# Performance work log

Hardware: AMD Instinct MI355X
Metric: run time of the kernel (lower is better)

Reference implementation:

```python
import jax, jax.numpy as jnp
import numpy as np

N_NODES = 100000
N_EDGES = 1600000
DIM = 128          # feat_dim == hidden_dim
N_LAYERS = 3
N_GRAPHS = 128
BN_EPS = 1e-5


def setup_inputs() -> dict:
    key = jax.random.key(0)
    ks = jax.random.split(key, 10)
    x = jax.random.normal(ks[0], (N_NODES, DIM), dtype=jnp.float32)
    edge_index = jax.random.randint(ks[1], (2, N_EDGES), 0, N_NODES, dtype=jnp.int32)
    batch = jnp.sort(jax.random.randint(ks[2], (N_NODES,), 0, N_GRAPHS, dtype=jnp.int32))
    # Xavier-uniform MLP weights (Linear stored as [in, out]); biases zero-init per module.
    a = float(np.sqrt(6.0 / (DIM + DIM)))
    W1 = jax.random.uniform(ks[3], (N_LAYERS, DIM, DIM), jnp.float32, -a, a)
    b1 = jnp.zeros((N_LAYERS, DIM), jnp.float32)
    W2 = jax.random.uniform(ks[4], (N_LAYERS, DIM, DIM), jnp.float32, -a, a)
    b2 = jnp.zeros((N_LAYERS, DIM), jnp.float32)
    gamma = jnp.ones((N_LAYERS, DIM), jnp.float32)   # BatchNorm weight
    beta = jnp.zeros((N_LAYERS, DIM), jnp.float32)   # BatchNorm bias
    return {"x": x, "edge_index": edge_index, "batch": batch,
            "W1": W1, "b1": b1, "W2": W2, "b2": b2, "gamma": gamma, "beta": beta}


def reference(x, edge_index, batch, W1, b1, W2, b2, gamma, beta):
    n_nodes = x.shape[0]
    src, dst = edge_index[0], edge_index[1]
    h = x
    xs = []
    for i in range(N_LAYERS):
        # GINConv (eps=0): h_i <- MLP((1+eps)*h_i + sum_{j->i} h_j)
        agg = jax.ops.segment_sum(h[src], dst, num_segments=n_nodes)
        z = h + agg
        z = jax.nn.relu(z @ W1[i] + b1[i]) @ W2[i] + b2[i]
        z = jax.nn.relu(z)
        # BatchNorm1d, training mode: biased batch stats over node dim
        mu = jnp.mean(z, axis=0)
        var = jnp.var(z, axis=0)
        h = gamma[i] * (z - mu) * jax.lax.rsqrt(var + BN_EPS) + beta[i]
        xs.append(h)
    # global_add_pool per layer output, concatenated over feature dim
    xpool = [jax.ops.segment_sum(xi, batch, num_segments=N_GRAPHS) for xi in xs]
    global_rep = jnp.concatenate(xpool, axis=1)  # [N_GRAPHS, N_LAYERS*DIM]
    return (global_rep, h)
```

## Files before the change

### kernel.cpp

```cpp
#include <hip/hip_runtime.h>

#define DIM 128
#define NLAYERS 3
#define NGRAPHS 128
#define BN_EPS 1e-5f
#define NSTAT 32

typedef __attribute__((ext_vector_type(8))) short short8v;
typedef __attribute__((ext_vector_type(8))) unsigned short ushort8v;
typedef __attribute__((ext_vector_type(4))) float f32x4;

__device__ __forceinline__ unsigned short f2bf(float f) {
  unsigned int x = __float_as_uint(f);
  unsigned int r = (x + 0x7fffu + ((x >> 16) & 1u)) >> 16;
  return (unsigned short)r;
}
__device__ __forceinline__ float bflo(unsigned int u) { return __uint_as_float(u << 16); }
__device__ __forceinline__ float bfhi(unsigned int u) { return __uint_as_float(u & 0xffff0000u); }
__device__ __forceinline__ float bf2f(unsigned short u) {
  return __uint_as_float(((unsigned int)u) << 16);
}


#define P1CH 4096

__global__ __launch_bounds__(256) void p1_kernel(const int* __restrict__ src,
                                                 const int* __restrict__ dst,
                                                 int* __restrict__ bucketCursor,
                                                 unsigned int* __restrict__ pairs,
                                                 int stride, int E, int NB) {
  __shared__ int cnt[128];
  __shared__ int base[128];
  int t = threadIdx.x;
  int e0 = blockIdx.x * P1CH;
  int e1 = min(e0 + P1CH, E);
  if (t < NB) cnt[t] = 0;
  __syncthreads();
  for (int e = e0 + t; e < e1; e += 256) atomicAdd(&cnt[dst[e] >> 10], 1);
  __syncthreads();
  if (t < NB) {
    base[t] = atomicAdd(&bucketCursor[t], cnt[t]);
    cnt[t] = 0;
  }
  __syncthreads();
  for (int e = e0 + t; e < e1; e += 256) {
    int d = dst[e];
    int b = d >> 10;
    int p = atomicAdd(&cnt[b], 1) + base[b];
    pairs[(size_t)b * stride + p] = ((unsigned int)(d & 1023) << 20) | (unsigned int)src[e];
  }
}

__global__ __launch_bounds__(128) void bscan2_kernel(const int* __restrict__ bucketCursor,
                                                     int* __restrict__ bucketBase,
                                                     int* __restrict__ offsets, int NB, int N) {
  __shared__ int p[128];
  int t = threadIdx.x;
  p[t] = (t < NB) ? bucketCursor[t] : 0;
  __syncthreads();
  for (int off = 1; off < 128; off <<= 1) {
    int v = (t >= off) ? p[t - off] : 0;
    __syncthreads();
    p[t] += v;
    __syncthreads();
  }
  if (t < NB) bucketBase[t] = (t == 0) ? 0 : p[t - 1];
  if (t == 0) offsets[N] = p[127];
}

__global__ __launch_bounds__(1024) void p2_kernel(const unsigned int* __restrict__ pairs,
                                                  const int* __restrict__ bucketCursor,
                                                  const int* __restrict__ bucketBase,
                                                  int stride, int* __restrict__ offsets,
                                                  int* __restrict__ eidx, int N) {
  __shared__ int cur[1024];
  int b = blockIdx.x;
  int t = threadIdx.x;
  int sz = bucketCursor[b];
  int ebase = bucketBase[b];
  const unsigned int* pp = pairs + (size_t)b * stride;
  cur[t] = 0;
  __syncthreads();
  for (int i = t; i < sz; i += 1024) atomicAdd(&cur[pp[i] >> 20], 1);
  __syncthreads();
  int v = cur[t];
  __syncthreads();
  cur[t] = v;
  __syncthreads();
  for (int off = 1; off < 1024; off <<= 1) {
    int u = (t >= off) ? cur[t - off] : 0;
    __syncthreads();
    cur[t] += u;
    __syncthreads();
  }
  int excl = cur[t] - v;
  int node = b * 1024 + t;
  if (node < N) offsets[node] = ebase + excl;
  cur[t] = excl;
  __syncthreads();
  for (int i = t; i < sz; i += 1024) {
    unsigned int pv = pp[i];
    int p = atomicAdd(&cur[pv >> 20], 1);
    eidx[ebase + p] = (int)(pv & 0xFFFFFu);
  }
}


__global__ __launch_bounds__(256) void convx_kernel(const float* __restrict__ x,
                                                    unsigned short* __restrict__ out,
                                                    int nquads) {
  int i = blockIdx.x * 256 + threadIdx.x;
  if (i < nquads) {
    float4 v = ((const float4*)x)[i];
    ushort4 o;
    o.x = f2bf(v.x); o.y = f2bf(v.y); o.z = f2bf(v.z); o.w = f2bf(v.w);
    ((ushort4*)out)[i] = o;
  }
}

__global__ __launch_bounds__(256) void convw_kernel(const float* __restrict__ W1,
                                                    const float* __restrict__ W2,
                                                    unsigned short* __restrict__ Wt) {
  int m = blockIdx.x;
  const float* W = (m < 3) ? (W1 + (size_t)m * 16384) : (W2 + (size_t)(m - 3) * 16384);
  unsigned short* out = Wt + (size_t)m * 16384;
  __shared__ unsigned short t[128 * 130];
  for (int i = threadIdx.x; i < 16384; i += 256) {
    int k = i >> 7, n = i & 127;
    t[n * 130 + k] = f2bf(W[i]);
  }
  __syncthreads();
  for (int i = threadIdx.x; i < 16384; i += 256) {
    int n = i >> 7, k = i & 127;
    out[i] = t[n * 130 + k];
  }
}

__global__ __launch_bounds__(128) void cnt_kernel(const int* __restrict__ batch,
                                                  int* __restrict__ cntG, int N) {
  int g = threadIdx.x;
  int lo = 0, hi = N;
  while (lo < hi) { int mid = (lo + hi) >> 1; if (batch[mid] < g) lo = mid + 1; else hi = mid; }
  int a = lo;
  lo = 0; hi = N;
  while (lo < hi) { int mid = (lo + hi) >> 1; if (batch[mid] < g + 1) lo = mid + 1; else hi = mid; }
  cntG[g] = lo - a;
}


__global__ __launch_bounds__(128) void bnfold_kernel(const float* __restrict__ statsRaw,
                                                     const float* __restrict__ gammaL,
                                                     const float* __restrict__ betaL,
                                                     float invN, float* __restrict__ folded) {
  int d = threadIdx.x;
  float s = 0.f, q = 0.f;
#pragma unroll
  for (int k = 0; k < NSTAT; ++k) {
    s += statsRaw[k * 256 + d];
    q += statsRaw[k * 256 + 128 + d];
  }
  float mu = s * invN;
  float var = q * invN - mu * mu;
  float sc = gammaL[d] * rsqrtf(var + BN_EPS);
  folded[d] = sc;
  folded[128 + d] = betaL[d] - mu * sc;
}


__global__ __launch_bounds__(256) void agg_kernel(const unsigned short* __restrict__ uin,
                                                  const int* __restrict__ offsets,
                                                  const int* __restrict__ eidx,
                                                  unsigned short* __restrict__ zout,
                                                  const float* __restrict__ foldedPrev,
                                                  int isFirst, int N) {
  int wid = (blockIdx.x * 256 + threadIdx.x) >> 6;
  int lane = threadIdx.x & 63;
  if (wid >= N) return;
  float scx = 1.f, scy = 1.f, shx = 0.f, shy = 0.f;
  if (!isFirst) {
    int d0 = lane * 2;
    float2 scv = *(const float2*)&foldedPrev[d0];
    float2 shv = *(const float2*)&foldedPrev[128 + d0];
    scx = scv.x; scy = scv.y; shx = shv.x; shy = shv.y;
  }
  const unsigned int* h32 = (const unsigned int*)uin;
  unsigned int own = h32[(size_t)wid * 64 + lane];
  float ax = bflo(own), ay = bfhi(own);
  int beg = offsets[wid], end = offsets[wid + 1];
  int e = beg;
  for (; e + 7 < end; e += 8) {
    int s0 = eidx[e], s1 = eidx[e + 1], s2 = eidx[e + 2], s3 = eidx[e + 3];
    int s4 = eidx[e + 4], s5 = eidx[e + 5], s6 = eidx[e + 6], s7 = eidx[e + 7];
    unsigned int u0 = h32[(size_t)s0 * 64 + lane];
    unsigned int u1 = h32[(size_t)s1 * 64 + lane];
    unsigned int u2 = h32[(size_t)s2 * 64 + lane];
    unsigned int u3 = h32[(size_t)s3 * 64 + lane];
    unsigned int u4 = h32[(size_t)s4 * 64 + lane];
    unsigned int u5 = h32[(size_t)s5 * 64 + lane];
    unsigned int u6 = h32[(size_t)s6 * 64 + lane];
    unsigned int u7 = h32[(size_t)s7 * 64 + lane];
    ax += bflo(u0) + bflo(u1) + bflo(u2) + bflo(u3);
    ay += bfhi(u0) + bfhi(u1) + bfhi(u2) + bfhi(u3);
    ax += bflo(u4) + bflo(u5) + bflo(u6) + bflo(u7);
    ay += bfhi(u4) + bfhi(u5) + bfhi(u6) + bfhi(u7);
  }
  for (; e + 1 < end; e += 2) {
    int s0 = eidx[e], s1 = eidx[e + 1];
    unsigned int u0 = h32[(size_t)s0 * 64 + lane];
    unsigned int u1 = h32[(size_t)s1 * 64 + lane];
    ax += bflo(u0) + bflo(u1);
    ay += bfhi(u0) + bfhi(u1);
  }
  if (e < end) {
    unsigned int u0 = h32[(size_t)eidx[e] * 64 + lane];
    ax += bflo(u0);
    ay += bfhi(u0);
  }
  float degp1 = (float)(end - beg + 1);
  float zx = scx * ax + degp1 * shx;
  float zy = scy * ay + degp1 * shy;
  unsigned int packed = (unsigned int)f2bf(zx) | ((unsigned int)f2bf(zy) << 16);
  ((unsigned int*)zout)[(size_t)wid * 64 + lane] = packed;
}


__global__ __launch_bounds__(256) void mlp_pool_kernel(unsigned short* __restrict__ zio,
                                                       const int* __restrict__ batch,
                                                       const unsigned short* __restrict__ WtA,
                                                       const float* __restrict__ b1,
                                                       const unsigned short* __restrict__ WtB,
                                                       const float* __restrict__ b2,
                                                       float* __restrict__ statsCur,
                                                       float* __restrict__ poolU,
                                                       int poolcol, int N) {
  __shared__ unsigned short tt[64 * 136];
  __shared__ float sstat[256];
  __shared__ int batchLDS[64];
  const int tid = threadIdx.x;
  const int n0 = blockIdx.x * 64;
  const int w = tid >> 6;
  const int lane = tid & 63;
  const int l15 = lane & 15;
  const int eslot = lane >> 4;
  const int hi8 = eslot << 3;
  sstat[tid] = 0.f;
  if (tid < 64) batchLDS[tid] = (n0 + tid < N) ? batch[n0 + tid] : 0;
  __syncthreads();

  const int arow = n0 + w * 16 + l15;
  const bool avalid = arow < N;

  f32x4 acc[8];
#pragma unroll
  for (int nf = 0; nf < 8; ++nf) acc[nf] = (f32x4){0.f, 0.f, 0.f, 0.f};
#pragma unroll
  for (int kt = 0; kt < 4; ++kt) {
    int kk = kt * 32 + hi8;
    short8v a0 = {0, 0, 0, 0, 0, 0, 0, 0};
    if (avalid) a0 = *(const short8v*)&zio[(size_t)arow * 128 + kk];
#pragma unroll
    for (int nf = 0; nf < 8; ++nf) {
      short8v b = *(const short8v*)&WtA[(size_t)(nf * 16 + l15) * 128 + kk];
      acc[nf] = __builtin_amdgcn_mfma_f32_16x16x32_bf16(a0, b, acc[nf], 0, 0, 0);
    }
  }
#pragma unroll
  for (int nf = 0; nf < 8; ++nf) {
    float bv = b1[nf * 16 + l15];
    int col = nf * 16 + l15;
#pragma unroll
    for (int q = 0; q < 4; ++q) {
      int row = w * 16 + eslot * 4 + q;
      tt[row * 136 + col] = f2bf(fmaxf(acc[nf][q] + bv, 0.f));
    }
  }

#pragma unroll
  for (int nf = 0; nf < 8; ++nf) acc[nf] = (f32x4){0.f, 0.f, 0.f, 0.f};
#pragma unroll
  for (int kt = 0; kt < 4; ++kt) {
    int kk = kt * 32 + hi8;
    short8v a0 = *(const short8v*)&tt[(w * 16 + l15) * 136 + kk];
#pragma unroll
    for (int nf = 0; nf < 8; ++nf) {
      short8v b = *(const short8v*)&WtB[(size_t)(nf * 16 + l15) * 128 + kk];
      acc[nf] = __builtin_amdgcn_mfma_f32_16x16x32_bf16(a0, b, acc[nf], 0, 0, 0);
    }
  }

#pragma unroll
  for (int nf = 0; nf < 8; ++nf) {
    float bv = b2[nf * 16 + l15];
    int col = nf * 16 + l15;
    float sv = 0.f, sq = 0.f;
#pragma unroll
    for (int q = 0; q < 4; ++q) {
      int row = w * 16 + eslot * 4 + q;
      float u = fmaxf(acc[nf][q] + bv, 0.f);
      tt[row * 136 + col] = f2bf(u);
      float um = ((n0 + row) < N) ? u : 0.f;
      sv += um;
      sq += um * um;
    }
    sv += __shfl_xor(sv, 16); sv += __shfl_xor(sv, 32);
    sq += __shfl_xor(sq, 16); sq += __shfl_xor(sq, 32);
    if (lane < 16) {
      atomicAdd(&sstat[col], sv);
      atomicAdd(&sstat[128 + col], sq);
    }
  }

  for (int i = lane; i < 256; i += 64) {
    int r = w * 16 + (i >> 4), c8 = (i & 15) << 3;
    int node = n0 + r;
    if (node < N)
      *(ushort8v*)&zio[(size_t)node * 128 + c8] = *(const ushort8v*)&tt[r * 136 + c8];
  }
  __syncthreads();

  float* myStat = statsCur + ((blockIdx.x & (NSTAT - 1)) << 8);
  atomicAdd(&myStat[tid], sstat[tid]);
  int d = tid & 127, half = tid >> 7;
  int curg = -1;
  float accp = 0.f;
  for (int r = half; r < 64; r += 2) {
    if (n0 + r >= N) break;
    float uv = bf2f(tt[r * 136 + d]);
    int g = batchLDS[r];
    if (g != curg) {
      if (curg >= 0) atomicAdd(&poolU[(size_t)curg * (NLAYERS * DIM) + poolcol + d], accp);
      curg = g;
      accp = 0.f;
    }
    accp += uv;
  }
  if (curg >= 0) atomicAdd(&poolU[(size_t)curg * (NLAYERS * DIM) + poolcol + d], accp);
}


__global__ __launch_bounds__(256) void hwrite_kernel(const unsigned short* __restrict__ u,
                                                     const float* __restrict__ folded,
                                                     float* __restrict__ hout, int N) {
  __shared__ float scs[128], shs[128];
  if (threadIdx.x < 128) {
    scs[threadIdx.x] = folded[threadIdx.x];
    shs[threadIdx.x] = folded[128 + threadIdx.x];
  }
  __syncthreads();
  int i = blockIdx.x * 256 + threadIdx.x;
  if (i >= N * 16) return;
  int row = i >> 4, c8 = (i & 15) << 3;
  ushort8v v = *(const ushort8v*)&u[(size_t)row * 128 + c8];
  float4 o0, o1;
  o0.x = scs[c8 + 0] * bf2f((unsigned short)v[0]) + shs[c8 + 0];
  o0.y = scs[c8 + 1] * bf2f((unsigned short)v[1]) + shs[c8 + 1];
  o0.z = scs[c8 + 2] * bf2f((unsigned short)v[2]) + shs[c8 + 2];
  o0.w = scs[c8 + 3] * bf2f((unsigned short)v[3]) + shs[c8 + 3];
  o1.x = scs[c8 + 4] * bf2f((unsigned short)v[4]) + shs[c8 + 4];
  o1.y = scs[c8 + 5] * bf2f((unsigned short)v[5]) + shs[c8 + 5];
  o1.z = scs[c8 + 6] * bf2f((unsigned short)v[6]) + shs[c8 + 6];
  o1.w = scs[c8 + 7] * bf2f((unsigned short)v[7]) + shs[c8 + 7];
  *(float4*)&hout[(size_t)row * 128 + c8] = o0;
  *(float4*)&hout[(size_t)row * 128 + c8 + 4] = o1;
}


__global__ __launch_bounds__(384) void pfin_kernel(const float* __restrict__ poolU,
                                                   const float* __restrict__ folded,
                                                   const int* __restrict__ cntG,
                                                   float* __restrict__ pool) {
  int g = blockIdx.x;
  int c = threadIdx.x;
  int L = c >> 7, d = c & 127;
  float sc = folded[L * 256 + d];
  float sh = folded[L * 256 + 128 + d];
  pool[(size_t)g * 384 + c] = sc * poolU[(size_t)g * 384 + c] + (float)cntG[g] * sh;
}


extern "C" void kernel_launch(void* const* d_in, const int* in_sizes, int n_in,
                              void* d_out, int out_size, void* d_ws, size_t ws_size,
                              hipStream_t stream) {
  const float* x = (const float*)d_in[0];
  const int* edge = (const int*)d_in[1];
  const int* batch = (const int*)d_in[2];
  const float* W1 = (const float*)d_in[3];
  const float* b1 = (const float*)d_in[4];
  const float* W2 = (const float*)d_in[5];
  const float* b2 = (const float*)d_in[6];
  const float* gamma = (const float*)d_in[7];
  const float* beta = (const float*)d_in[8];

  int N = in_sizes[0] / DIM;
  int E = in_sizes[1] / 2;
  const int* src = edge;
  const int* dst = edge + E;
  int NB = (N + 1023) >> 10;
  int stride = E / NB + E / (NB * 4) + 2048;

  const int statsSz = NLAYERS * NSTAT * 256;
  char* w = (char*)d_ws;
  int* eidx = (int*)w;                w += sizeof(int) * (size_t)E;
  int* offsets = (int*)w;             w += sizeof(int) * (size_t)(N + 8);
  int* bucketCursor = (int*)w;        w += sizeof(int) * 128;
  int* bucketBase = (int*)w;          w += sizeof(int) * 128;
  float* gstats = (float*)w;          w += sizeof(float) * statsSz;
  float* folded = (float*)w;          w += sizeof(float) * NLAYERS * 256;
  float* poolU = (float*)w;           w += sizeof(float) * (size_t)NGRAPHS * NLAYERS * DIM;
  int* cntG = (int*)w;                w += sizeof(int) * 128;
  unsigned short* Wt = (unsigned short*)w;  w += sizeof(short) * 6 * 16384;
  uintptr_t a = ((uintptr_t)w + 255) & ~(uintptr_t)255;
  unsigned short* bufA = (unsigned short*)a;
  unsigned short* bufB = bufA + (size_t)N * 128;
  unsigned int* pairs = (unsigned int*)bufA;

  float* pool = (float*)d_out;
  float* hout = (float*)d_out + (size_t)NGRAPHS * NLAYERS * DIM;

  hipMemsetAsync(bucketCursor, 0, 128 * sizeof(int), stream);
  hipMemsetAsync(gstats, 0,
                 (statsSz + NLAYERS * 256 + (size_t)NGRAPHS * NLAYERS * DIM) * sizeof(float),
                 stream);

  convw_kernel<<<6, 256, 0, stream>>>(W1, W2, Wt);
  convx_kernel<<<(N * DIM / 4 + 255) / 256, 256, 0, stream>>>(x, bufB, N * DIM / 4);

  p1_kernel<<<(E + P1CH - 1) / P1CH, 256, 0, stream>>>(src, dst, bucketCursor, pairs,
                                                       stride, E, NB);
  bscan2_kernel<<<1, 128, 0, stream>>>(bucketCursor, bucketBase, offsets, NB, N);
  p2_kernel<<<NB, 1024, 0, stream>>>(pairs, bucketCursor, bucketBase, stride, offsets,
                                     eidx, N);
  cnt_kernel<<<1, 128, 0, stream>>>(batch, cntG, N);

  float invN = 1.0f / (float)N;
  int ablk = (N + 3) / 4;
  int mblk = (N + 63) / 64;
  float* st0 = gstats;
  float* st1 = gstats + NSTAT * 256;
  float* st2 = gstats + 2 * NSTAT * 256;

  agg_kernel<<<ablk, 256, 0, stream>>>(bufB, offsets, eidx, bufA, folded, 1, N);
  mlp_pool_kernel<<<mblk, 256, 0, stream>>>(bufA, batch, Wt + 0 * 16384, b1 + 0,
                                            Wt + 3 * 16384, b2 + 0, st0, poolU, 0, N);
  bnfold_kernel<<<1, 128, 0, stream>>>(st0, gamma + 0, beta + 0, invN, folded + 0);
  agg_kernel<<<ablk, 256, 0, stream>>>(bufA, offsets, eidx, bufB, folded + 0, 0, N);
  mlp_pool_kernel<<<mblk, 256, 0, stream>>>(bufB, batch, Wt + 1 * 16384, b1 + 128,
                                            Wt + 4 * 16384, b2 + 128, st1, poolU, 128, N);
  bnfold_kernel<<<1, 128, 0, stream>>>(st1, gamma + 128, beta + 128, invN, folded + 256);
  agg_kernel<<<ablk, 256, 0, stream>>>(bufB, offsets, eidx, bufA, folded + 256, 0, N);
  mlp_pool_kernel<<<mblk, 256, 0, stream>>>(bufA, batch, Wt + 2 * 16384, b1 + 256,
                                            Wt + 5 * 16384, b2 + 256, st2, poolU, 256, N);
  bnfold_kernel<<<1, 128, 0, stream>>>(st2, gamma + 256, beta + 256, invN, folded + 512);

  hwrite_kernel<<<(N * 16 + 255) / 256, 256, 0, stream>>>(bufA, folded + 512, hout, N);
  pfin_kernel<<<NGRAPHS, 384, 0, stream>>>(poolU, folded, cntG, pool);
}
```

Baseline: 519.0 us.

## Split MLP into per-wave 64-row GEMM kernel and separate pool/stats kernel

The fused MLP+pool kernel is split in two. The GEMM kernel gives each wave 64 rows and holds the weight fragments in registers across four row tiles, so weight loads are reused instead of reloaded per 16 rows. A separate kernel then reads the bf16 output back to compute the BatchNorm statistics and the graph pooling, and the stats slot count is doubled to reduce atomic contention. This costs one extra launch and an extra full read of the activations per layer, and the larger accumulator array raises register pressure.

```diff
diff --git a/kernel.cpp b/kernel.cpp
--- a/kernel.cpp
+++ b/kernel.cpp
@@ -4,7 +4,7 @@
 #define NLAYERS 3
 #define NGRAPHS 128
 #define BN_EPS 1e-5f
-#define NSTAT 32
+#define NSTAT 64
 
 typedef __attribute__((ext_vector_type(8))) short short8v;
 typedef __attribute__((ext_vector_type(8))) unsigned short ushort8v;
@@ -224,117 +224,149 @@
 }
 
 
-__global__ __launch_bounds__(256) void mlp_pool_kernel(unsigned short* __restrict__ zio,
-                                                       const int* __restrict__ batch,
+__global__ __launch_bounds__(128) void mlp_gemm_kernel(unsigned short* __restrict__ zio,
                                                        const unsigned short* __restrict__ WtA,
                                                        const float* __restrict__ b1,
                                                        const unsigned short* __restrict__ WtB,
-                                                       const float* __restrict__ b2,
-                                                       float* __restrict__ statsCur,
-                                                       float* __restrict__ poolU,
-                                                       int poolcol, int N) {
-  __shared__ unsigned short tt[64 * 136];
-  __shared__ float sstat[256];
-  __shared__ int batchLDS[64];
+                                                       const float* __restrict__ b2, int N) {
+  __shared__ unsigned short tt[2][64 * 136];
   const int tid = threadIdx.x;
-  const int n0 = blockIdx.x * 64;
-  const int w = tid >> 6;
+  const int wv = tid >> 6;
   const int lane = tid & 63;
   const int l15 = lane & 15;
   const int eslot = lane >> 4;
-  const int hi8 = eslot << 3;
-  sstat[tid] = 0.f;
-  if (tid < 64) batchLDS[tid] = (n0 + tid < N) ? batch[n0 + tid] : 0;
-  __syncthreads();
-
-  const int arow = n0 + w * 16 + l15;
-  const bool avalid = arow < N;
-
-  f32x4 acc[8];
-#pragma unroll
-  for (int nf = 0; nf < 8; ++nf) acc[nf] = (f32x4){0.f, 0.f, 0.f, 0.f};
-#pragma unroll
+  const int wid = blockIdx.x * 2 + wv;
+  const int n0 = wid * 64;
+  if (n0 >= N) return;
+  unsigned short* t = tt[wv];
+
+  f32x4 acc[4][8];
+#pragma unroll
+  for (int rt = 0; rt < 4; ++rt)
+#pragma unroll
+    for (int nf = 0; nf < 8; ++nf) acc[rt][nf] = (f32x4){0.f, 0.f, 0.f, 0.f};
   for (int kt = 0; kt < 4; ++kt) {
-    int kk = kt * 32 + hi8;
-    short8v a0 = {0, 0, 0, 0, 0, 0, 0, 0};
-    if (avalid) a0 = *(const short8v*)&zio[(size_t)arow * 128 + kk];
+    int kk = kt * 32 + eslot * 8;
+    short8v b[8];
+#pragma unroll
+    for (int nf = 0; nf < 8; ++nf)
+      b[nf] = *(const short8v*)&WtA[(size_t)(nf * 16 + l15) * 128 + kk];
+#pragma unroll
+    for (int rt = 0; rt < 4; ++rt) {
+      int arow = n0 + rt * 16 + l15;
+      short8v a = {0, 0, 0, 0, 0, 0, 0, 0};
+      if (arow < N) a = *(const short8v*)&zio[(size_t)arow * 128 + kk];
+#pragma unroll
+      for (int nf = 0; nf < 8; ++nf)
+        acc[rt][nf] = __builtin_amdgcn_mfma_f32_16x16x32_bf16(a, b[nf], acc[rt][nf], 0, 0, 0);
+    }
+  }
+#pragma unroll
+  for (int rt = 0; rt < 4; ++rt)
 #pragma unroll
     for (int nf = 0; nf < 8; ++nf) {
-      short8v b = *(const short8v*)&WtA[(size_t)(nf * 16 + l15) * 128 + kk];
-      acc[nf] = __builtin_amdgcn_mfma_f32_16x16x32_bf16(a0, b, acc[nf], 0, 0, 0);
+      float bv = b1[nf * 16 + l15];
+      int col = nf * 16 + l15;
+#pragma unroll
+      for (int q = 0; q < 4; ++q) {
+        int row = rt * 16 + eslot * 4 + q;
+        t[row * 136 + col] = f2bf(fmaxf(acc[rt][nf][q] + bv, 0.f));
+      }
     }
-  }
-#pragma unroll
-  for (int nf = 0; nf < 8; ++nf) {
-    float bv = b1[nf * 16 + l15];
-    int col = nf * 16 + l15;
-#pragma unroll
-    for (int q = 0; q < 4; ++q) {
-      int row = w * 16 + eslot * 4 + q;
-      tt[row * 136 + col] = f2bf(fmaxf(acc[nf][q] + bv, 0.f));
+
+#pragma unroll
+  for (int rt = 0; rt < 4; ++rt)
+#pragma unroll
+    for (int nf = 0; nf < 8; ++nf) acc[rt][nf] = (f32x4){0.f, 0.f, 0.f, 0.f};
+  for (int kt = 0; kt < 4; ++kt) {
+    int kk = kt * 32 + eslot * 8;
+    short8v b[8];
+#pragma unroll
+    for (int nf = 0; nf < 8; ++nf)
+      b[nf] = *(const short8v*)&WtB[(size_t)(nf * 16 + l15) * 128 + kk];
+#pragma unroll
+    for (int rt = 0; rt < 4; ++rt) {
+      short8v a = *(const short8v*)&t[(rt * 16 + l15) * 136 + kk];
+#pragma unroll
+      for (int nf = 0; nf < 8; ++nf)
+        acc[rt][nf] = __builtin_amdgcn_mfma_f32_16x16x32_bf16(a, b[nf], acc[rt][nf], 0, 0, 0);
     }
   }
-
-#pragma unroll
-  for (int nf = 0; nf < 8; ++nf) acc[nf] = (f32x4){0.f, 0.f, 0.f, 0.f};
-#pragma unroll
-  for (int kt = 0; kt < 4; ++kt) {
-    int kk = kt * 32 + hi8;
-    short8v a0 = *(const short8v*)&tt[(w * 16 + l15) * 136 + kk];
+#pragma unroll
+  for (int rt = 0; rt < 4; ++rt)
 #pragma unroll
     for (int nf = 0; nf < 8; ++nf) {
-      short8v b = *(const short8v*)&WtB[(size_t)(nf * 16 + l15) * 128 + kk];
-      acc[nf] = __builtin_amdgcn_mfma_f32_16x16x32_bf16(a0, b, acc[nf], 0, 0, 0);
+      float bv = b2[nf * 16 + l15];
+      int col = nf * 16 + l15;
+#pragma unroll
+      for (int q = 0; q < 4; ++q) {
+        int row = rt * 16 + eslot * 4 + q;
+        t[row * 136 + col] = f2bf(fmaxf(acc[rt][nf][q] + bv, 0.f));
+      }
     }
-  }
-
-#pragma unroll
-  for (int nf = 0; nf < 8; ++nf) {
-    float bv = b2[nf * 16 + l15];
-    int col = nf * 16 + l15;
-    float sv = 0.f, sq = 0.f;
-#pragma unroll
-    for (int q = 0; q < 4; ++q) {
-      int row = w * 16 + eslot * 4 + q;
-      float u = fmaxf(acc[nf][q] + bv, 0.f);
-      tt[row * 136 + col] = f2bf(u);
-      float um = ((n0 + row) < N) ? u : 0.f;
-      sv += um;
-      sq += um * um;
-    }
-    sv += __shfl_xor(sv, 16); sv += __shfl_xor(sv, 32);
-    sq += __shfl_xor(sq, 16); sq += __shfl_xor(sq, 32);
-    if (lane < 16) {
-      atomicAdd(&sstat[col], sv);
-      atomicAdd(&sstat[128 + col], sq);
-    }
-  }
-
-  for (int i = lane; i < 256; i += 64) {
-    int r = w * 16 + (i >> 4), c8 = (i & 15) << 3;
+
+  for (int i = lane; i < 1024; i += 64) {
+    int r = i >> 4, c8 = (i & 15) << 3;
     int node = n0 + r;
     if (node < N)
-      *(ushort8v*)&zio[(size_t)node * 128 + c8] = *(const ushort8v*)&tt[r * 136 + c8];
-  }
-  __syncthreads();
-
-  float* myStat = statsCur + ((blockIdx.x & (NSTAT - 1)) << 8);
-  atomicAdd(&myStat[tid], sstat[tid]);
-  int d = tid & 127, half = tid >> 7;
+      *(ushort8v*)&zio[(size_t)node * 128 + c8] = *(const ushort8v*)&t[r * 136 + c8];
+  }
+}
+
+
+__global__ __launch_bounds__(256) void pool_stats_kernel(const unsigned short* __restrict__ u,
+                                                         const int* __restrict__ batch,
+                                                         float* __restrict__ statsCur,
+                                                         float* __restrict__ poolU,
+                                                         int poolcol, int N) {
+  __shared__ float sstat[512];
+  __shared__ int batchLDS[128];
+  const int tid = threadIdx.x;
+  const int n0 = blockIdx.x * 128;
+  sstat[tid] = 0.f;
+  sstat[tid + 256] = 0.f;
+  if (tid < 128) batchLDS[tid] = (n0 + tid < N) ? batch[n0 + tid] : 0;
+  __syncthreads();
+
+  const int dh = tid & 63;
+  const int rg = tid >> 6;
+  const int dp = dh * 2;
+  const unsigned int* u32p = (const unsigned int*)u;
+  float s0 = 0.f, s1 = 0.f, q0 = 0.f, q1 = 0.f;
   int curg = -1;
-  float accp = 0.f;
-  for (int r = half; r < 64; r += 2) {
-    if (n0 + r >= N) break;
-    float uv = bf2f(tt[r * 136 + d]);
+  float a0 = 0.f, a1 = 0.f;
+  for (int r = rg; r < 128; r += 4) {
+    int node = n0 + r;
+    if (node >= N) break;
+    unsigned int v = u32p[(size_t)node * 64 + dh];
+    float x0 = bflo(v), x1 = bfhi(v);
+    s0 += x0; s1 += x1;
+    q0 += x0 * x0; q1 += x1 * x1;
     int g = batchLDS[r];
     if (g != curg) {
-      if (curg >= 0) atomicAdd(&poolU[(size_t)curg * (NLAYERS * DIM) + poolcol + d], accp);
+      if (curg >= 0) {
+        atomicAdd(&poolU[(size_t)curg * (NLAYERS * DIM) + poolcol + dp], a0);
+        atomicAdd(&poolU[(size_t)curg * (NLAYERS * DIM) + poolcol + dp + 1], a1);
+      }
       curg = g;
-      accp = 0.f;
+      a0 = 0.f; a1 = 0.f;
     }
-    accp += uv;
-  }
-  if (curg >= 0) atomicAdd(&poolU[(size_t)curg * (NLAYERS * DIM) + poolcol + d], accp);
+    a0 += x0; a1 += x1;
+  }
+  if (curg >= 0) {
+    atomicAdd(&poolU[(size_t)curg * (NLAYERS * DIM) + poolcol + dp], a0);
+    atomicAdd(&poolU[(size_t)curg * (NLAYERS * DIM) + poolcol + dp + 1], a1);
+  }
+  atomicAdd(&sstat[dp], s0);
+  atomicAdd(&sstat[dp + 1], s1);
+  atomicAdd(&sstat[256 + dp], q0);
+  atomicAdd(&sstat[256 + dp + 1], q1);
+  __syncthreads();
+  float* myStat = statsCur + ((blockIdx.x & (NSTAT - 1)) << 8);
+  if (tid < 128) {
+    atomicAdd(&myStat[tid], sstat[tid]);
+    atomicAdd(&myStat[128 + tid], sstat[256 + tid]);
+  }
 }
 
 
@@ -434,22 +466,26 @@
 
   float invN = 1.0f / (float)N;
   int ablk = (N + 3) / 4;
-  int mblk = (N + 63) / 64;
+  int gblk = (N + 127) / 128;
+  int pblk = (N + 127) / 128;
   float* st0 = gstats;
   float* st1 = gstats + NSTAT * 256;
   float* st2 = gstats + 2 * NSTAT * 256;
 
   agg_kernel<<<ablk, 256, 0, stream>>>(bufB, offsets, eidx, bufA, folded, 1, N);
-  mlp_pool_kernel<<<mblk, 256, 0, stream>>>(bufA, batch, Wt + 0 * 16384, b1 + 0,
-                                            Wt + 3 * 16384, b2 + 0, st0, poolU, 0, N);
+  mlp_gemm_kernel<<<gblk, 128, 0, stream>>>(bufA, Wt + 0 * 16384, b1 + 0,
+                                            Wt + 3 * 16384, b2 + 0, N);
+  pool_stats_kernel<<<pblk, 256, 0, stream>>>(bufA, batch, st0, poolU, 0, N);
   bnfold_kernel<<<1, 128, 0, stream>>>(st0, gamma + 0, beta + 0, invN, folded + 0);
   agg_kernel<<<ablk, 256, 0, stream>>>(bufA, offsets, eidx, bufB, folded + 0, 0, N);
-  mlp_pool_kernel<<<mblk, 256, 0, stream>>>(bufB, batch, Wt + 1 * 16384, b1 + 128,
-                                            Wt + 4 * 16384, b2 + 128, st1, poolU, 128, N);
+  mlp_gemm_kernel<<<gblk, 128, 0, stream>>>(bufB, Wt + 1 * 16384, b1 + 128,
+                                            Wt + 4 * 16384, b2 + 128, N);
+  pool_stats_kernel<<<pblk, 256, 0, stream>>>(bufB, batch, st1, poolU, 128, N);
   bnfold_kernel<<<1, 128, 0, stream>>>(st1, gamma + 128, beta + 128, invN, folded + 256);
   agg_kernel<<<ablk, 256, 0, stream>>>(bufB, offsets, eidx, bufA, folded + 256, 0, N);
-  mlp_pool_kernel<<<mblk, 256, 0, stream>>>(bufA, batch, Wt + 2 * 16384, b1 + 256,
-                                            Wt + 5 * 16384, b2 + 256, st2, poolU, 256, N);
+  mlp_gemm_kernel<<<gblk, 128, 0, stream>>>(bufA, Wt + 2 * 16384, b1 + 256,
+                                            Wt + 5 * 16384, b2 + 256, N);
+  pool_stats_kernel<<<pblk, 256, 0, stream>>>(bufA, batch, st2, poolU, 256, N);
   bnfold_kernel<<<1, 128, 0, stream>>>(st2, gamma + 256, beta + 256, invN, folded + 512);
 
   hwrite_kernel<<<(N * 16 + 255) / 256, 256, 0, stream>>>(bufA, folded + 512, hout, N);
```

After: 453.3 us. 12.7% less time.
